# Kernel tuning notes

Measured on AMD Instinct MI355X. Metric: run time of the kernel, lower is better.

The kernel has to match this reference:

```python
import jax, jax.numpy as jnp
import numpy as np
import math

B, S, D, H = 4, 1024, 1024, 16
DK = D // H


def setup_inputs() -> dict:
    key = jax.random.key(0)
    ks = jax.random.split(key, 12)
    scale = 1.0 / math.sqrt(D)
    inp = {
        "query": jax.random.normal(ks[0], (B, S, D), jnp.float32),
        "key": jax.random.normal(ks[1], (B, S, D), jnp.float32),
        "value": jax.random.normal(ks[2], (B, S, D), jnp.float32),
        "mask": jnp.ones((B, S, S), jnp.int32),
        "Wq": jax.random.uniform(ks[3], (D, D), jnp.float32, -scale, scale),
        "bq": jax.random.uniform(ks[4], (D,), jnp.float32, -scale, scale),
        "Wk": jax.random.uniform(ks[5], (D, D), jnp.float32, -scale, scale),
        "bk": jax.random.uniform(ks[6], (D,), jnp.float32, -scale, scale),
        "Wv": jax.random.uniform(ks[7], (D, D), jnp.float32, -scale, scale),
        "bv": jax.random.uniform(ks[8], (D,), jnp.float32, -scale, scale),
        "Wo": jax.random.uniform(ks[9], (D, D), jnp.float32, -scale, scale),
        "bo": jax.random.uniform(ks[10], (D,), jnp.float32, -scale, scale),
    }
    return inp


def reference(query, key, value, mask, Wq, bq, Wk, bk, Wv, bv, Wo, bo):
    b, s, d = query.shape
    # QKV projections (torch Linear: x @ W.T + b), split into heads -> [b, h, s, dk]
    def proj(x, W, bias):
        return (x @ W.T + bias).reshape(b, -1, H, DK).transpose(0, 2, 1, 3)

    q = proj(query, Wq, bq)
    k = proj(key, Wk, bk)
    v = proj(value, Wv, bv)

    scores = jnp.einsum("bhqd,bhkd->bhqk", q, k) / jnp.sqrt(jnp.float32(DK))
    scores = jnp.where(mask[:, None, :, :] == 0, jnp.float32(-1e9), scores)
    p_attn = jax.nn.softmax(scores, axis=-1)  # dropout p=0.0 -> identity

    x = jnp.einsum("bhqk,bhkd->bhqd", p_attn, v)
    x = x.transpose(0, 2, 1, 3).reshape(b, -1, H * DK)  # [b, s, d]
    # F.threshold(x, 0.2, 0.0): values <= 0.2 replaced with 0
    x = jnp.where(x > 0.2, x, jnp.float32(0.0))
    x1 = x @ Wo.T + bo
    x1 = jnp.mean(x1, axis=-1, keepdims=True)
    return x + x1
```

## Files before the change

kernel.cpp:

```cpp
#include <hip/hip_runtime.h>
#include <hip/hip_bf16.h>
#include <math.h>

#define BB 4
#define SS 1024
#define DD 1024
#define NH 16
#define DKH 64

typedef __attribute__((ext_vector_type(8))) short bf16x8;
typedef __attribute__((ext_vector_type(4))) float f32x4;
typedef __attribute__((ext_vector_type(16))) float f32x16;

__device__ __forceinline__ ushort f2bf(float f) {
  __hip_bfloat16 h = __float2bfloat16(f);
  return *(ushort*)&h;
}

__device__ __forceinline__ bf16x8 pack8(float4 a, float4 b) {
  bf16x8 r;
  r[0] = (short)f2bf(a.x); r[1] = (short)f2bf(a.y);
  r[2] = (short)f2bf(a.z); r[3] = (short)f2bf(a.w);
  r[4] = (short)f2bf(b.x); r[5] = (short)f2bf(b.y);
  r[6] = (short)f2bf(b.z); r[7] = (short)f2bf(b.w);
  return r;
}

__device__ __forceinline__ void async16(const void* g, void* l) {
  __builtin_amdgcn_global_load_lds(
      (const __attribute__((address_space(1))) unsigned int*)g,
      (__attribute__((address_space(3))) unsigned int*)l, 16, 0, 0);
}

__global__ __launch_bounds__(256) void prep_all(
    const float* __restrict__ Xq, const float* __restrict__ Xk, const float* __restrict__ Xv,
    const int* __restrict__ mask,
    const float* __restrict__ Wq, const float* __restrict__ Wk, const float* __restrict__ Wv,
    const float* __restrict__ Wo, const float* __restrict__ bo,
    ushort* __restrict__ Wb, ushort* __restrict__ Ab,
    float* __restrict__ wo_sum, float* __restrict__ bo_mean,
    int* __restrict__ maskOK) {
  __shared__ int smi[4];
  const int bid = blockIdx.x;
  const int tid = threadIdx.x;

  if (bid < 64) {
    const int row0 = bid * 16;
    const int c = (tid + bid * 4) & 255;
    float4 acc = make_float4(0.f, 0.f, 0.f, 0.f);
#pragma unroll
    for (int r = 0; r < 16; ++r) {
      const float4 v = *(const float4*)(Wo + (size_t)(row0 + r) * DD + c * 4);
      acc.x += v.x; acc.y += v.y; acc.z += v.z; acc.w += v.w;
    }
    atomicAdd(&wo_sum[c * 4 + 0], acc.x);
    atomicAdd(&wo_sum[c * 4 + 1], acc.y);
    atomicAdd(&wo_sum[c * 4 + 2], acc.z);
    atomicAdd(&wo_sum[c * 4 + 3], acc.w);
    return;
  }

  if (bid == 64) {
    if (tid < 64) {
      float s = 0.f;
      for (int i = tid; i < 1024; i += 64) s += bo[i];
#pragma unroll
      for (int off = 1; off < 64; off <<= 1) s += __shfl_xor(s, off);
      if (tid == 0) *bo_mean = s * (1.0f / 1024.0f);
    }
    return;
  }

  if (bid < 577) {
    const int m = bid - 65;
    const int kt = m & 15, qt = (m >> 4) & 7, b = m >> 7;
    const int row = tid >> 1, half = tid & 1;
    const int* p = mask + ((size_t)b * SS + qt * 128 + row) * SS + kt * 64 + half * 32;
    int ok = 1;
#pragma unroll
    for (int j = 0; j < 8; ++j) {
      const int4 mm = *(const int4*)(p + j * 4);
      ok &= (mm.x != 0) & (mm.y != 0) & (mm.z != 0) & (mm.w != 0);
    }
    const unsigned long long bal = __ballot(ok);
    if ((tid & 63) == 0) smi[tid >> 6] = (bal == ~0ULL) ? 1 : 0;
    __syncthreads();
    if (tid == 0) maskOK[(b * 8 + qt) * 16 + kt] = smi[0] & smi[1] & smi[2] & smi[3];
    return;
  }

  if (bid < 1345) {
    const int c0 = bid - 577;
#pragma unroll
    for (int it = 0; it < 8; ++it) {
      const size_t g = (size_t)(c0 + it * 768) * 2048 + (size_t)tid * 8;
      const int t = (int)(g >> 22);
      const float* base = (t == 0) ? Xq : (t == 1) ? Xk : Xv;
      const size_t off = g & 4194303;
      const float4 f0 = *(const float4*)(base + off);
      const float4 f1 = *(const float4*)(base + off + 4);
      *(bf16x8*)(Ab + g) = pack8(f0, f1);
    }
    return;
  }

  {
    const int c0 = bid - 1345;
#pragma unroll
    for (int it = 0; it < 8; ++it) {
      const size_t g = (size_t)(c0 + it * 192) * 2048 + (size_t)tid * 8;
      const int t = (int)(g >> 20);
      const float* W = (t == 0) ? Wq : (t == 1) ? Wk : Wv;
      const size_t off = g & 1048575;
      const float4 f0 = *(const float4*)(W + off);
      const float4 f1 = *(const float4*)(W + off + 4);
      *(bf16x8*)(Wb + g) = pack8(f0, f1);
    }
  }
}

__global__ __launch_bounds__(256) void gemm_qkv_bf16(
    const ushort* __restrict__ Ab, const ushort* __restrict__ Wb,
    const float* __restrict__ bq, const float* __restrict__ bk, const float* __restrict__ bv,
    ushort* __restrict__ QKVb) {
  const int z = blockIdx.z;
  const char* A = (const char*)(Ab + (size_t)z * 4194304);
  const char* W = (const char*)(Wb + (size_t)z * 1048576);
  const float* bias = (z == 0) ? bq : (z == 1) ? bk : bv;
  ushort* Cz = QKVb + (size_t)z * 4194304;
  const float scale = (z == 0) ? 0.125f : 1.0f;

  __shared__ ushort As[8192];
  __shared__ ushort Ws[8192];

  const int tid = threadIdx.x;
  const int lane = tid & 63, w = tid >> 6;
  const int l31 = lane & 31, kh = lane >> 5;
  const int wn = w & 1, wm = w >> 1;
  const int m0 = blockIdx.x * 128, n0 = blockIdx.y * 128;

  const int r8 = lane >> 3;
  const int cg = (lane & 7) ^ r8;
  const int xr = l31 & 7;

  f32x16 acc[2][2];
#pragma unroll
  for (int mt = 0; mt < 2; ++mt)
#pragma unroll
    for (int nt = 0; nt < 2; ++nt)
#pragma unroll
      for (int r = 0; r < 16; ++r) acc[mt][nt][r] = 0.f;

  for (int k0 = 0; k0 < DD; k0 += 64) {
    __syncthreads();
#pragma unroll
    for (int t = 0; t < 4; ++t) {
      const int grp = w * 4 + t;
      const int row = grp * 8 + r8;
      async16(A + ((size_t)(m0 + row) * DD + k0 + cg * 8) * 2, &As[grp * 512]);
      async16(W + ((size_t)(n0 + row) * DD + k0 + cg * 8) * 2, &Ws[grp * 512]);
    }
    __syncthreads();
#pragma unroll
    for (int ks = 0; ks < 4; ++ks) {
      const int sc = (ks * 2 + kh) ^ xr;
      bf16x8 wf[2], af[2];
#pragma unroll
      for (int nt = 0; nt < 2; ++nt)
        wf[nt] = *(const bf16x8*)&Ws[(wn * 64 + nt * 32 + l31) * 64 + sc * 8];
#pragma unroll
      for (int mt = 0; mt < 2; ++mt)
        af[mt] = *(const bf16x8*)&As[(wm * 64 + mt * 32 + l31) * 64 + sc * 8];
#pragma unroll
      for (int mt = 0; mt < 2; ++mt)
#pragma unroll
        for (int nt = 0; nt < 2; ++nt)
          acc[mt][nt] = __builtin_amdgcn_mfma_f32_32x32x16_bf16(wf[nt], af[mt], acc[mt][nt], 0, 0, 0);
    }
  }

  const int hh = blockIdx.y * 2 + wn;
#pragma unroll
  for (int nt = 0; nt < 2; ++nt) {
#pragma unroll
    for (int g = 0; g < 4; ++g) {
      const int ng = n0 + wn * 64 + nt * 32 + kh * 4 + g * 8;
      const int d = nt * 32 + kh * 4 + g * 8;
      const float4 b4 = *(const float4*)(bias + ng);
#pragma unroll
      for (int mt = 0; mt < 2; ++mt) {
        const int row = m0 + wm * 64 + mt * 32 + l31;
        ushort4 pk;
        pk.x = f2bf((acc[mt][nt][g * 4 + 0] + b4.x) * scale);
        pk.y = f2bf((acc[mt][nt][g * 4 + 1] + b4.y) * scale);
        pk.z = f2bf((acc[mt][nt][g * 4 + 2] + b4.z) * scale);
        pk.w = f2bf((acc[mt][nt][g * 4 + 3] + b4.w) * scale);
        *(ushort4*)&Cz[(size_t)hh * 262144 + (size_t)row * 64 + d] = pk;
      }
    }
  }
}

__global__ __launch_bounds__(256) void flash_mfma(
    const ushort* __restrict__ QKVb, const int* __restrict__ mask,
    const int* __restrict__ maskOK, float* __restrict__ X) {
  __shared__ ushort Ks[2][4096];
  __shared__ ushort Vt[64 * 72];
  __shared__ ushort Ps[128 * 72];

  const int tid = threadIdx.x;
  const int lane = tid & 63, w = tid >> 6;
  const int quad = lane >> 4, l15 = lane & 15;
  const int h = blockIdx.x, qblk = blockIdx.y, b = blockIdx.z;
  const int qbase = qblk * 128 + w * 32;

  const ushort* Qh = QKVb + (size_t)h * 262144;
  const ushort* Kh = QKVb + 4194304 + (size_t)h * 262144 + (size_t)(b * SS) * 64;
  const ushort* Vh = QKVb + 8388608 + (size_t)h * 262144 + (size_t)(b * SS) * 64;

  bf16x8 qf[2][2];
#pragma unroll
  for (int qt = 0; qt < 2; ++qt)
#pragma unroll
    for (int ks = 0; ks < 2; ++ks)
      qf[qt][ks] = *(const bf16x8*)(Qh + (size_t)(b * SS + qbase + qt * 16 + l15) * 64 +
                                    ks * 32 + quad * 8);

  unsigned okbits = 0;
  {
    const int* mkp = maskOK + (b * 8 + qblk) * 16;
#pragma unroll
    for (int i = 0; i < 16; ++i) okbits |= (mkp[i] ? 1u : 0u) << i;
  }

  f32x4 o[4][2];
  const f32x4 z4 = {0.f, 0.f, 0.f, 0.f};
#pragma unroll
  for (int dt = 0; dt < 4; ++dt)
#pragma unroll
    for (int qt = 0; qt < 2; ++qt) o[dt][qt] = z4;
  float l_run[2] = {0.f, 0.f};

  const int vp = tid & 31;
  const int vdc = tid >> 5;
  const ushort* Vg = Vh + vdc * 8;
  uint* VtU = (uint*)Vt;
  const int* Mb = mask + (size_t)b * SS * SS;

  const int r8k = tid >> 3;
  const int gk = (tid & 7) ^ (r8k & 7);
  const int xk = l15 & 7;

  union U8 { uint4 u; ushort s[8]; };

  async16(Kh + (size_t)r8k * 64 + gk * 8, &Ks[0][(size_t)tid * 8]);
  async16(Kh + (size_t)(32 + r8k) * 64 + gk * 8, &Ks[0][2048 + (size_t)tid * 8]);
  U8 v0c, v1c;
  v0c.u = *(const uint4*)(Vg + (size_t)(2 * vp) * 64);
  v1c.u = *(const uint4*)(Vg + (size_t)(2 * vp + 1) * 64);

  for (int kt = 0; kt < 16; ++kt) {
    const int k064 = kt * 64;
    const int cur = kt & 1;

    __builtin_amdgcn_s_barrier();
#pragma unroll
    for (int j = 0; j < 8; ++j)
      VtU[(vdc * 8 + j) * 36 + vp] = (uint)v0c.s[j] | ((uint)v1c.s[j] << 16);
    if (kt < 15) {
      const ushort* Kt = Kh + (size_t)(k064 + 64) * 64;
      async16(Kt + (size_t)r8k * 64 + gk * 8, &Ks[cur ^ 1][(size_t)tid * 8]);
      async16(Kt + (size_t)(32 + r8k) * 64 + gk * 8, &Ks[cur ^ 1][2048 + (size_t)tid * 8]);
    }
    asm volatile("s_waitcnt lgkmcnt(0)" ::: "memory");
    __builtin_amdgcn_sched_barrier(0);
    __builtin_amdgcn_s_barrier();

    const int kn = (kt < 15) ? (k064 + 64) : 0;
    U8 v0n, v1n;
    v0n.u = *(const uint4*)(Vg + (size_t)(kn + 2 * vp) * 64);
    v1n.u = *(const uint4*)(Vg + (size_t)(kn + 2 * vp + 1) * 64);

    f32x4 s[4][2];
    __builtin_amdgcn_s_setprio(1);
#pragma unroll
    for (int mt = 0; mt < 4; ++mt) {
      const int rr = mt * 16 + l15;
      bf16x8 kf0 = *(const bf16x8*)&Ks[cur][rr * 64 + ((quad) ^ xk) * 8];
      bf16x8 kf1 = *(const bf16x8*)&Ks[cur][rr * 64 + ((4 + quad) ^ xk) * 8];
#pragma unroll
      for (int qt = 0; qt < 2; ++qt) {
        f32x4 a = z4;
        a = __builtin_amdgcn_mfma_f32_16x16x32_bf16(kf0, qf[qt][0], a, 0, 0, 0);
        a = __builtin_amdgcn_mfma_f32_16x16x32_bf16(kf1, qf[qt][1], a, 0, 0, 0);
        s[mt][qt] = a;
      }
    }
    __builtin_amdgcn_s_setprio(0);

    if (!((okbits >> kt) & 1)) {
#pragma unroll
      for (int mt = 0; mt < 4; ++mt)
#pragma unroll
        for (int qt = 0; qt < 2; ++qt)
#pragma unroll
          for (int reg = 0; reg < 4; ++reg) {
            const int q = qbase + qt * 16 + l15;
            const int key = k064 + mt * 16 + quad * 4 + reg;
            if (Mb[(size_t)q * SS + key] == 0) s[mt][qt][reg] = -1e9f;
          }
    }

#pragma unroll
    for (int qt = 0; qt < 2; ++qt) {
      float rs = 0.f;
#pragma unroll
      for (int mt = 0; mt < 4; ++mt) {
#pragma unroll
        for (int reg = 0; reg < 4; ++reg) {
          const float p = __expf(s[mt][qt][reg]);
          s[mt][qt][reg] = p;
          rs += p;
        }
      }
      l_run[qt] += rs;
#pragma unroll
      for (int mt = 0; mt < 4; ++mt) {
        ushort4 pk;
        pk.x = f2bf(s[mt][qt][0]);
        pk.y = f2bf(s[mt][qt][1]);
        pk.z = f2bf(s[mt][qt][2]);
        pk.w = f2bf(s[mt][qt][3]);
        *(ushort4*)&Ps[(w * 32 + qt * 16 + l15) * 72 + mt * 16 + quad * 4] = pk;
      }
    }

    bf16x8 pf[2][2];
#pragma unroll
    for (int qt = 0; qt < 2; ++qt)
#pragma unroll
      for (int ks = 0; ks < 2; ++ks)
        pf[qt][ks] = *(const bf16x8*)&Ps[(w * 32 + qt * 16 + l15) * 72 + ks * 32 + quad * 8];
    __builtin_amdgcn_s_setprio(1);
#pragma unroll
    for (int dt = 0; dt < 4; ++dt) {
      bf16x8 vf0 = *(const bf16x8*)&Vt[(dt * 16 + l15) * 72 + quad * 8];
      bf16x8 vf1 = *(const bf16x8*)&Vt[(dt * 16 + l15) * 72 + 32 + quad * 8];
#pragma unroll
      for (int qt = 0; qt < 2; ++qt) {
        o[dt][qt] = __builtin_amdgcn_mfma_f32_16x16x32_bf16(vf0, pf[qt][0], o[dt][qt], 0, 0, 0);
        o[dt][qt] = __builtin_amdgcn_mfma_f32_16x16x32_bf16(vf1, pf[qt][1], o[dt][qt], 0, 0, 0);
      }
    }
    __builtin_amdgcn_s_setprio(0);

    v0c.u = v0n.u;
    v1c.u = v1n.u;
  }

#pragma unroll
  for (int qt = 0; qt < 2; ++qt) {
    float l = l_run[qt];
    l += __shfl_xor(l, 16);
    l += __shfl_xor(l, 32);
    const float inv = 1.0f / l;
#pragma unroll
    for (int dt = 0; dt < 4; ++dt) {
      const f32x4 ov = o[dt][qt] * inv;
      *(f32x4*)(X + (size_t)(b * SS + qbase + qt * 16 + l15) * DD +
                h * DKH + dt * 16 + quad * 4) = ov;
    }
  }
}

__global__ __launch_bounds__(256) void epilogue_kernel(float* __restrict__ X,
                                                       const float* __restrict__ wo_sum,
                                                       const float* __restrict__ bo_mean) {
  __shared__ float red[4][4];
  const int tid = threadIdx.x;
  const float4 wv = *(const float4*)(wo_sum + tid * 4);
  const float bm = *bo_mean;
  float4 xt[4];
#pragma unroll
  for (int r = 0; r < 4; ++r) {
    const int row = blockIdx.x * 4 + r;
    const float4 x = *(const float4*)(X + (size_t)row * DD + tid * 4);
    xt[r].x = (x.x > 0.2f) ? x.x : 0.f;
    xt[r].y = (x.y > 0.2f) ? x.y : 0.f;
    xt[r].z = (x.z > 0.2f) ? x.z : 0.f;
    xt[r].w = (x.w > 0.2f) ? x.w : 0.f;
    float part = xt[r].x * wv.x + xt[r].y * wv.y + xt[r].z * wv.z + xt[r].w * wv.w;
#pragma unroll
    for (int off = 1; off < 64; off <<= 1) part += __shfl_xor(part, off);
    if ((tid & 63) == 0) red[r][tid >> 6] = part;
  }
  __syncthreads();
#pragma unroll
  for (int r = 0; r < 4; ++r) {
    const int row = blockIdx.x * 4 + r;
    const float x1 = ((red[r][0] + red[r][1]) + (red[r][2] + red[r][3])) * (1.0f / 1024.0f) + bm;
    const float4 o = make_float4(xt[r].x + x1, xt[r].y + x1, xt[r].z + x1, xt[r].w + x1);
    *(float4*)(X + (size_t)row * DD + tid * 4) = o;
  }
}

extern "C" void kernel_launch(void* const* d_in, const int* in_sizes, int n_in,
                              void* d_out, int out_size, void* d_ws, size_t ws_size,
                              hipStream_t stream) {
  const float* Xq = (const float*)d_in[0];
  const float* Xk = (const float*)d_in[1];
  const float* Xv = (const float*)d_in[2];
  const int* mask = (const int*)d_in[3];
  const float* Wq = (const float*)d_in[4];
  const float* bq = (const float*)d_in[5];
  const float* Wk = (const float*)d_in[6];
  const float* bk = (const float*)d_in[7];
  const float* Wv = (const float*)d_in[8];
  const float* bv = (const float*)d_in[9];
  const float* Wo = (const float*)d_in[10];
  const float* bo = (const float*)d_in[11];

  ushort* Wb = (ushort*)d_ws;
  ushort* Ab = Wb + (size_t)3 * 1048576;
  ushort* QKVb = Ab + (size_t)3 * 4194304;
  float* wo_sum = (float*)(QKVb + (size_t)3 * 4194304);
  float* bo_mean = wo_sum + 1024;
  int* maskOK = (int*)(bo_mean + 1);
  float* X = (float*)d_out;

  hipMemsetAsync(wo_sum, 0, 1024 * sizeof(float), stream);

  prep_all<<<1537, 256, 0, stream>>>(Xq, Xk, Xv, mask, Wq, Wk, Wv, Wo, bo,
                                     Wb, Ab, wo_sum, bo_mean, maskOK);

  gemm_qkv_bf16<<<dim3(32, 8, 3), 256, 0, stream>>>(Ab, Wb, bq, bk, bv, QKVb);

  flash_mfma<<<dim3(16, 8, 4), 256, 0, stream>>>(QKVb, mask, maskOK, X);

  epilogue_kernel<<<1024, 256, 0, stream>>>(X, wo_sum, bo_mean);
}
```

Before: 214.8 us.

## Double-buffer QKV GEMM shared tiles with smaller K step and new swizzle

Splits the QKV projection GEMM's shared-memory tiles into two K=32 buffers and prefetches the next slice asynchronously while MFMAs run on the current one. This replaces the K=64 single-buffer loop that had two barriers per iteration. Shared-memory reads use a new row-rotation swizzle to avoid bank conflicts. The loop now has one barrier per iteration but twice as many iterations. Correctness depends on the async loads completing before that barrier.

```diff
diff --git a/kernel.cpp b/kernel.cpp
--- a/kernel.cpp
+++ b/kernel.cpp
@@ -130,8 +130,8 @@
   ushort* Cz = QKVb + (size_t)z * 4194304;
   const float scale = (z == 0) ? 0.125f : 1.0f;
 
-  __shared__ ushort As[8192];
-  __shared__ ushort Ws[8192];
+  __shared__ ushort As[2][4096];
+  __shared__ ushort Ws[2][4096];
 
   const int tid = threadIdx.x;
   const int lane = tid & 63, w = tid >> 6;
@@ -139,9 +139,10 @@
   const int wn = w & 1, wm = w >> 1;
   const int m0 = blockIdx.x * 128, n0 = blockIdx.y * 128;
 
-  const int r8 = lane >> 3;
-  const int cg = (lane & 7) ^ r8;
-  const int xr = l31 & 7;
+  const int rowA = tid >> 2;
+  const int cA = ((tid & 3) - ((rowA >> 1) & 3)) & 3;
+  const int rowB = 64 + (tid >> 2);
+  const int cB = ((tid & 3) - ((rowB >> 1) & 3)) & 3;
 
   f32x16 acc[2][2];
 #pragma unroll
@@ -151,32 +152,43 @@
 #pragma unroll
       for (int r = 0; r < 16; ++r) acc[mt][nt][r] = 0.f;
 
-  for (int k0 = 0; k0 < DD; k0 += 64) {
-    __syncthreads();
-#pragma unroll
-    for (int t = 0; t < 4; ++t) {
-      const int grp = w * 4 + t;
-      const int row = grp * 8 + r8;
-      async16(A + ((size_t)(m0 + row) * DD + k0 + cg * 8) * 2, &As[grp * 512]);
-      async16(W + ((size_t)(n0 + row) * DD + k0 + cg * 8) * 2, &Ws[grp * 512]);
-    }
-    __syncthreads();
-#pragma unroll
-    for (int ks = 0; ks < 4; ++ks) {
-      const int sc = (ks * 2 + kh) ^ xr;
+  async16(A + ((size_t)(m0 + rowA) * DD + cA * 8) * 2, &As[0][tid * 8]);
+  async16(W + ((size_t)(n0 + rowA) * DD + cA * 8) * 2, &Ws[0][tid * 8]);
+  async16(A + ((size_t)(m0 + rowB) * DD + cB * 8) * 2, &As[0][2048 + tid * 8]);
+  async16(W + ((size_t)(n0 + rowB) * DD + cB * 8) * 2, &Ws[0][2048 + tid * 8]);
+  __syncthreads();
+
+  for (int i = 0; i < 32; ++i) {
+    const int cur = i & 1;
+    if (i < 31) {
+      const int k0n = (i + 1) * 32;
+      async16(A + ((size_t)(m0 + rowA) * DD + k0n + cA * 8) * 2, &As[cur ^ 1][tid * 8]);
+      async16(W + ((size_t)(n0 + rowA) * DD + k0n + cA * 8) * 2, &Ws[cur ^ 1][tid * 8]);
+      async16(A + ((size_t)(m0 + rowB) * DD + k0n + cB * 8) * 2, &As[cur ^ 1][2048 + tid * 8]);
+      async16(W + ((size_t)(n0 + rowB) * DD + k0n + cB * 8) * 2, &Ws[cur ^ 1][2048 + tid * 8]);
+    }
+#pragma unroll
+    for (int ks = 0; ks < 2; ++ks) {
       bf16x8 wf[2], af[2];
 #pragma unroll
-      for (int nt = 0; nt < 2; ++nt)
-        wf[nt] = *(const bf16x8*)&Ws[(wn * 64 + nt * 32 + l31) * 64 + sc * 8];
-#pragma unroll
-      for (int mt = 0; mt < 2; ++mt)
-        af[mt] = *(const bf16x8*)&As[(wm * 64 + mt * 32 + l31) * 64 + sc * 8];
+      for (int nt = 0; nt < 2; ++nt) {
+        const int r = wn * 64 + nt * 32 + l31;
+        const int s = (ks * 2 + kh + ((r >> 1) & 3)) & 3;
+        wf[nt] = *(const bf16x8*)&Ws[cur][r * 32 + s * 8];
+      }
+#pragma unroll
+      for (int mt = 0; mt < 2; ++mt) {
+        const int r = wm * 64 + mt * 32 + l31;
+        const int s = (ks * 2 + kh + ((r >> 1) & 3)) & 3;
+        af[mt] = *(const bf16x8*)&As[cur][r * 32 + s * 8];
+      }
 #pragma unroll
       for (int mt = 0; mt < 2; ++mt)
 #pragma unroll
         for (int nt = 0; nt < 2; ++nt)
           acc[mt][nt] = __builtin_amdgcn_mfma_f32_32x32x16_bf16(wf[nt], af[mt], acc[mt][nt], 0, 0, 0);
     }
+    __syncthreads();
   }
 
   const int hh = blockIdx.y * 2 + wn;
```

Result: no change. 214.5 us (median of 3 runs) (-0.1%).
